# Optimization experiments

Measured on AMD Instinct MI355X. Metric: run time of the kernel, lower is better.

Reference implementation:

```python
import jax, jax.numpy as jnp
import numpy as np

B, S, C, DM, NH, DH = 1, 2048, 2048, 768, 12, 64
LN_EPS = 1e-9


def setup_inputs() -> dict:
    rng = jax.random.key(0)
    ks = jax.random.split(rng, 24)
    f32 = jnp.float32
    p = 0.02  # param init scale
    inp = {
        'query': jax.random.normal(ks[0], (B, S, DM), f32),
        'key': jax.random.normal(ks[1], (B, C, DM), f32),
        'value': jax.random.normal(ks[2], (B, C, DM), f32),
        'phi': jax.random.normal(ks[3], (S, DM), f32) * p,
        'pi': jax.random.normal(ks[4], (S, DM), f32) * p,
        'psi': jax.random.normal(ks[5], (C, DM), f32) * p,
        'omega': jax.random.normal(ks[6], (C, DM), f32) * p,
        'cls_mask': jnp.ones((S, C), f32),
        'token_type_mat': jax.random.randint(ks[7], (B, S, C), 0, 2).astype(bool),
        'attention_mask': jnp.ones((B, C), jnp.int32),
        # learned parameters
        'Wq': jax.random.normal(ks[8], (DM, NH * DH), f32) * p,
        'Wk': jax.random.normal(ks[9], (DM, NH * DH), f32) * p,
        'bk': jnp.zeros((NH * DH,), f32),
        'Wv': jax.random.normal(ks[10], (DM, NH * DH), f32) * p,
        'bv': jnp.zeros((NH * DH,), f32),
        'r_w_bias': jax.random.normal(ks[11], (NH, DH), f32) * p,
        'r_r_bias': jax.random.normal(ks[12], (NH, DH), f32) * p,
        'r_kernel': jax.random.normal(ks[13], (DM, NH, DH), f32) * p,
        'r_s_bias': jax.random.normal(ks[14], (NH, DH), f32) * p,
        'seg_embed': jax.random.normal(ks[15], (2, NH, DH), f32) * p,
        'Wo': jax.random.normal(ks[16], (NH * DH, DM), f32) * p,
        'bo': jnp.zeros((DM,), f32),
        'ln_scale': jnp.ones((DM,), f32),
        'ln_bias': jnp.zeros((DM,), f32),
    }
    return inp


def reference(query, key, value, phi, pi, psi, omega, cls_mask,
              token_type_mat, attention_mask,
              Wq, Wk, bk, Wv, bv, r_w_bias, r_r_bias, r_kernel,
              r_s_bias, seg_embed, Wo, bo, ln_scale, ln_bias):
    b, s, _ = query.shape
    c = key.shape[1]
    scale = 1.0 / DH ** 0.5
    # head projections
    q = (query @ Wq).reshape(b, s, NH, DH) * scale          # [b,i,n,h]
    k = (key @ Wk + bk).reshape(b, c, NH, DH)                # [b,j,n,h]
    v = (value @ Wv + bv).reshape(b, c, NH, DH)
    # content score
    content = jnp.einsum('binh,bjnh->bnij', q + r_w_bias * scale, k)
    # factorized relative positional attention
    qr = jnp.einsum('binh,dnh->bind', q + r_r_bias * scale, r_kernel)  # [b,i,n,d_model]
    pos = (jnp.einsum('bind,jd->bnij', qr * phi[:, None], psi)
           + jnp.einsum('bind,jd->bnij', qr * pi[:, None], omega))
    pos = pos * cls_mask
    # token-type attention
    tt_bias = jnp.einsum('binh,snh->bnis', q + r_s_bias * scale, seg_embed)  # [b,n,i,2]
    diff_tt, same_tt = jnp.split(tt_bias, 2, axis=-1)  # each [b,n,i,1]
    tt = jnp.where(token_type_mat[:, None], same_tt, diff_tt) * cls_mask
    # combine, mask, softmax
    score = content + pos + tt
    score = score - 1000000.0 * (1.0 - attention_mask[:, None, None].astype(jnp.float32))
    prob = jax.nn.softmax(score, axis=-1)  # [b,n,i,j]
    attn_vec = jnp.einsum('bnij,bjnh->binh', prob, v).reshape(b, s, NH * DH)
    attn_out = attn_vec @ Wo + bo
    # residual + layernorm
    x = query + attn_out
    mu = x.mean(-1, keepdims=True)
    var = x.var(-1, keepdims=True)
    return (x - mu) * jax.lax.rsqrt(var + LN_EPS) * ln_scale + ln_bias
```

## Files before the change

kernel.cpp:

```cpp
#include <hip/hip_runtime.h>
#include <hip/hip_bf16.h>
#include <stddef.h>

#define DEVINL __device__ __forceinline__

typedef __attribute__((ext_vector_type(8))) short short8;
typedef __attribute__((ext_vector_type(4))) float f32x4;

static constexpr int S_LEN = 2048;
static constexpr int C_LEN = 2048;
static constexpr int DMODEL = 768;
static constexpr int NHEAD = 12;
static constexpr int DHEAD = 64;
static constexpr float SCALE = 0.125f;

DEVINL float bf2f(short s) {
    union { unsigned u; float f; } v;
    v.u = ((unsigned)(unsigned short)s) << 16;
    return v.f;
}
DEVINL short f2bf(float f) {
    union { float f; unsigned u; } v;
    v.f = f;
    unsigned r = v.u + 0x7FFFu + ((v.u >> 16) & 1u);
    return (short)(r >> 16);
}
DEVINL f32x4 zero4() { f32x4 z; z[0]=0.f; z[1]=0.f; z[2]=0.f; z[3]=0.f; return z; }

DEVINL int swz(int width, int row, int col) {
    return (row * width + col) ^ ((row & 7) << 3);
}

DEVINL void gl_lds16(const short* g, short* l) {
    __builtin_amdgcn_global_load_lds(
        (const __attribute__((address_space(1))) void*)g,
        (__attribute__((address_space(3))) void*)l,
        16, 0, 0);
}

template<int ROWS, int WIDTH>
DEVINL void stage_lds_swz(short* lds_tile, const short* src, int src_stride, int w, int lane) {
    constexpr int CPR = WIDTH / 8;
    constexpr int CH  = ROWS * CPR;
    for (int c0 = w * 64; c0 < CH; c0 += 256) {
        int chunk = c0 + lane;
        int row   = chunk / CPR;
        int ccol  = chunk % CPR;
        int scol  = ccol ^ (row & 7);
        gl_lds16(src + (size_t)row * src_stride + scol * 8, lds_tile + c0 * 8);
    }
}

DEVINL void stage_addcol(short* dst, const short* src, const float* p1, const float* p2,
                         int col0, int src_stride) {
    for (int c = threadIdx.x; c < 1024; c += 256) {
        int row = c >> 3;
        int cc  = (c & 7) * 8;
        short8 a = *(const short8*)(src + (size_t)row * src_stride + cc);
        short8 r;
#pragma unroll
        for (int e = 0; e < 8; ++e)
            r[e] = f2bf(bf2f(a[e]) + (p1[col0 + cc + e] - p2[col0 + cc + e]) * SCALE);
        *(short8*)(dst + swz(64, row, cc)) = r;
    }
}

DEVINL void mfma_step_128(const short* As, const short* Bs, f32x4 acc[4][4],
                          int wr, int wc, int lane) {
#pragma unroll
    for (int kk = 0; kk < 64; kk += 32) {
        short8 a[4], b[4];
#pragma unroll
        for (int mi = 0; mi < 4; ++mi)
            a[mi] = *(const short8*)(As + swz(64, wr*64 + mi*16 + (lane & 15), kk + (lane >> 4) * 8));
#pragma unroll
        for (int ni = 0; ni < 4; ++ni)
            b[ni] = *(const short8*)(Bs + swz(64, wc*64 + ni*16 + (lane & 15), kk + (lane >> 4) * 8));
#pragma unroll
        for (int mi = 0; mi < 4; ++mi)
#pragma unroll
            for (int ni = 0; ni < 4; ++ni)
                acc[mi][ni] = __builtin_amdgcn_mfma_f32_16x16x32_bf16(a[mi], b[ni], acc[mi][ni], 0, 0, 0);
    }
}

DEVINL void mfma_row16(const short* As, const short* Bs, f32x4 acc[8], int w, int lane) {
#pragma unroll
    for (int kk = 0; kk < 64; kk += 32) {
        short8 a = *(const short8*)(As + swz(64, w*16 + (lane & 15), kk + (lane >> 4) * 8));
#pragma unroll
        for (int nj = 0; nj < 8; ++nj) {
            short8 b = *(const short8*)(Bs + swz(64, nj*16 + (lane & 15), kk + (lane >> 4) * 8));
            acc[nj] = __builtin_amdgcn_mfma_f32_16x16x32_bf16(a, b, acc[nj], 0, 0, 0);
        }
    }
}

template<int KSTEPS>
DEVINL void gemm128_body(const short* A, const short* Bt, short* As, short* Bs,
                         f32x4 acc[4][4], int wr, int wc, int lane, int w) {
    for (int ks = 0; ks < KSTEPS; ++ks) {
        if (ks) __syncthreads();
        stage_lds_swz<128, 64>(As, A + ks * 64, DMODEL, w, lane);
        stage_lds_swz<128, 64>(Bs, Bt + ks * 64, DMODEL, w, lane);
        __syncthreads();
        mfma_step_128(As, Bs, acc, wr, wc, lane);
    }
}

__global__ void conv_kernel(const float* q, const float* k, const float* v,
                            const float* psi, const float* omega, const float* rk,
                            short* qc, short* kc, short* vc,
                            short* psc, short* omc, short* rkc) {
    int z = blockIdx.z;
    const float* src; short* dst; int n4;
    switch (z) {
        case 0: src = q;     dst = qc;  n4 = 393216; break;
        case 1: src = k;     dst = kc;  n4 = 393216; break;
        case 2: src = v;     dst = vc;  n4 = 393216; break;
        case 3: src = psi;   dst = psc; n4 = 393216; break;
        case 4: src = omega; dst = omc; n4 = 393216; break;
        default: src = rk;   dst = rkc; n4 = 147456; break;
    }
    for (int i = blockIdx.x * 256 + threadIdx.x; i < n4; i += gridDim.x * 256) {
        float4 f = *(const float4*)(src + (size_t)i * 4);
        short4 o;
        o.x = f2bf(f.x); o.y = f2bf(f.y); o.z = f2bf(f.z); o.w = f2bf(f.w);
        *(short4*)(dst + (size_t)i * 4) = o;
    }
}

__global__ void transpose_kernel(const float* wq, const float* wk, const float* wv, const float* wo,
                                 short* wqt, short* wkt, short* wvt, short* wot) {
    __shared__ float tile[64][65];
    int z = blockIdx.z;
    const float* src = (z == 0) ? wq : (z == 1) ? wk : (z == 2) ? wv : wo;
    short*       dst = (z == 0) ? wqt : (z == 1) ? wkt : (z == 2) ? wvt : wot;
    int r0 = blockIdx.x * 64, c0 = blockIdx.y * 64;
    for (int e = threadIdx.x; e < 4096; e += 256) {
        int rr = e >> 6, cc = e & 63;
        tile[rr][cc] = src[(size_t)(r0 + rr) * DMODEL + c0 + cc];
    }
    __syncthreads();
    for (int e = threadIdx.x; e < 4096; e += 256) {
        int rr = e >> 6, cc = e & 63;
        dst[(size_t)(c0 + rr) * DMODEL + r0 + cc] = f2bf(tile[cc][rr]);
    }
}

__global__ __launch_bounds__(256, 2)
void qkv_kernel(const short* qc, const short* kc, const short* vc,
                const short* wqt, const short* wkt, const short* wvt,
                const float* bk, const float* bv, const float* rw,
                short* qw_a, short* kpack, short* vt) {
    __shared__ short As[128 * 64], Bs[128 * 64];
    int z = blockIdx.z;
    const short* A  = (z == 0) ? qc  : (z == 1) ? kc  : vc;
    const short* Bt = (z == 0) ? wqt : (z == 1) ? wkt : wvt;
    int i0 = blockIdx.x * 128, c0 = blockIdx.y * 128;
    int t = threadIdx.x, lane = t & 63, w = t >> 6, wr = w >> 1, wc = w & 1;

    f32x4 acc[4][4];
#pragma unroll
    for (int mi = 0; mi < 4; ++mi)
#pragma unroll
        for (int ni = 0; ni < 4; ++ni) acc[mi][ni] = zero4();

    gemm128_body<12>(A + (size_t)i0 * DMODEL, Bt + (size_t)c0 * DMODEL, As, Bs, acc, wr, wc, lane, w);

#pragma unroll
    for (int mi = 0; mi < 4; ++mi)
#pragma unroll
        for (int ni = 0; ni < 4; ++ni)
#pragma unroll
            for (int r = 0; r < 4; ++r) {
                int row = i0 + wr*64 + mi*16 + ((lane >> 4) << 2) + r;
                int col = c0 + wc*64 + ni*16 + (lane & 15);
                float v = acc[mi][ni][r];
                if (z == 0) {
                    qw_a[(size_t)row * DMODEL + col] = f2bf(v * SCALE + rw[col] * SCALE);
                } else if (z == 1) {
                    float vv = v + bk[col];
                    kpack[((size_t)(col >> 6) * C_LEN + row) * DHEAD + (col & 63)] = f2bf(vv);
                } else {
                    float vv = v + bv[col];
                    vt[((size_t)(col >> 6) * DHEAD + (col & 63)) * C_LEN + row] = f2bf(vv);
                }
            }
}

__global__ __launch_bounds__(256, 2)
void qr_kernel(const short* qwa, const short* rkc, const float* rr, const float* rw,
               const float* phi, const float* pi_, short* a1, short* a2, int n_base) {
    __shared__ short As[128 * 64], Bs[128 * 64];
    int nl = blockIdx.z, n = n_base + nl;
    int i0 = blockIdx.x * 128, d0 = blockIdx.y * 128;
    int t = threadIdx.x, lane = t & 63, w = t >> 6, wr = w >> 1, wc = w & 1;

    f32x4 acc[4][4];
#pragma unroll
    for (int mi = 0; mi < 4; ++mi)
#pragma unroll
        for (int ni = 0; ni < 4; ++ni) acc[mi][ni] = zero4();

    stage_addcol(As, qwa + (size_t)i0 * DMODEL + n * DHEAD, rr, rw, n * DHEAD, DMODEL);
    stage_lds_swz<128, 64>(Bs, rkc + (size_t)d0 * DMODEL + n * DHEAD, DMODEL, w, lane);
    __syncthreads();
    mfma_step_128(As, Bs, acc, wr, wc, lane);

#pragma unroll
    for (int mi = 0; mi < 4; ++mi)
#pragma unroll
        for (int ni = 0; ni < 4; ++ni)
#pragma unroll
            for (int r = 0; r < 4; ++r) {
                int row = i0 + wr*64 + mi*16 + ((lane >> 4) << 2) + r;
                int col = d0 + wc*64 + ni*16 + (lane & 15);
                float v = acc[mi][ni][r];
                size_t src = (size_t)row * DMODEL + col;
                size_t dst = ((size_t)nl * S_LEN + row) * DMODEL + col;
                a1[dst] = f2bf(v * phi[src]);
                a2[dst] = f2bf(v * pi_[src]);
            }
}

__global__ void ttb_kernel(const short* qwa, const float* seg, const float* rs, const float* rw,
                           float* ttd, float* tts) {
    int idx = blockIdx.x * 256 + threadIdx.x;
    int n = idx >> 11, i = idx & 2047;
    const short* q  = qwa + (size_t)i * DMODEL + n * DHEAD;
    const float* e0 = seg + n * DHEAD;
    const float* e1 = seg + NHEAD * DHEAD + n * DHEAD;
    float s0 = 0.f, s1 = 0.f;
#pragma unroll
    for (int h = 0; h < DHEAD; ++h) {
        float qv = bf2f(q[h]) + (rs[n * DHEAD + h] - rw[n * DHEAD + h]) * SCALE;
        s0 += qv * e0[h];
        s1 += qv * e1[h];
    }
    ttd[n * S_LEN + i] = s0;
    tts[n * S_LEN + i] = s1;
}

__global__ __launch_bounds__(256, 4)
void flash_kernel(const short* qw_a, const short* kpack, const short* a1, const short* a2,
                  const short* psc, const short* omc, const float* cls_mask,
                  const int* ttmat, const int* amask, const float* ttd, const float* tts,
                  const short* vt, short* pacc, float* pm, float* pl, int n_base) {
    __shared__ short As[64 * 64];
    __shared__ short Bs[128 * 64];
    __shared__ short Ps[64 * 128];

    int nl = blockIdx.y, n = n_base + nl;
    int i0 = blockIdx.x * 64;
    int jt = blockIdx.z;
    int j0 = jt * 128;
    int t = threadIdx.x, lane = t & 63, w = t >> 6;
    int lrow = lane >> 4;
    int lcol = lane & 15;

    f32x4 acc_c[8], acc_p[8];
#pragma unroll
    for (int nj = 0; nj < 8; ++nj) { acc_c[nj] = zero4(); acc_p[nj] = zero4(); }

    stage_lds_swz<64, 64>(As, qw_a + (size_t)i0 * DMODEL + n * DHEAD, DMODEL, w, lane);
    stage_lds_swz<128, 64>(Bs, kpack + ((size_t)n * C_LEN + j0) * DHEAD, DHEAD, w, lane);
    __syncthreads();
    mfma_row16(As, Bs, acc_c, w, lane);

    for (int ks = 0; ks < 24; ++ks) {
        int d0 = (ks % 12) * 64;
        const short* asrc = ((ks < 12) ? a1 : a2) + ((size_t)nl * S_LEN + i0) * DMODEL + d0;
        const short* bsrc = ((ks < 12) ? psc : omc) + (size_t)j0 * DMODEL + d0;
        __syncthreads();
        stage_lds_swz<64, 64>(As, asrc, DMODEL, w, lane);
        stage_lds_swz<128, 64>(Bs, bsrc, DMODEL, w, lane);
        __syncthreads();
        mfma_row16(As, Bs, acc_p, w, lane);
    }

    int iBase = i0 + w*16 + lrow*4;
    float tdiff[4], tsame[4];
#pragma unroll
    for (int r = 0; r < 4; ++r) {
        tdiff[r] = ttd[n * S_LEN + iBase + r];
        tsame[r] = tts[n * S_LEN + iBase + r];
    }
    float pbuf[8][4];
    float m[4] = { -1.0e9f, -1.0e9f, -1.0e9f, -1.0e9f };
#pragma unroll
    for (int nj = 0; nj < 8; ++nj) {
        int jg = j0 + nj*16 + lcol;
        float pen = 1.0e6f * (1.0f - (float)amask[jg]);
#pragma unroll
        for (int r = 0; r < 4; ++r) {
            size_t eidx = (size_t)(iBase + r) * C_LEN + jg;
            float clsv = cls_mask[eidx];
            float ttv  = ttmat[eidx] ? tsame[r] : tdiff[r];
            float sc = acc_c[nj][r] + clsv * (acc_p[nj][r] + ttv) - pen;
            pbuf[nj][r] = sc;
            m[r] = fmaxf(m[r], sc);
        }
    }
#pragma unroll
    for (int r = 0; r < 4; ++r) {
        float v = m[r];
        v = fmaxf(v, __shfl_xor(v, 1));
        v = fmaxf(v, __shfl_xor(v, 2));
        v = fmaxf(v, __shfl_xor(v, 4));
        v = fmaxf(v, __shfl_xor(v, 8));
        m[r] = v;
    }
    float l[4] = { 0.f, 0.f, 0.f, 0.f };
#pragma unroll
    for (int nj = 0; nj < 8; ++nj)
#pragma unroll
        for (int r = 0; r < 4; ++r) {
            float pv = __expf(fminf(pbuf[nj][r] - m[r], 0.0f));
            pbuf[nj][r] = pv;
            l[r] += pv;
        }
#pragma unroll
    for (int r = 0; r < 4; ++r) {
        float v = l[r];
        v += __shfl_xor(v, 1);
        v += __shfl_xor(v, 2);
        v += __shfl_xor(v, 4);
        v += __shfl_xor(v, 8);
        l[r] = v;
    }

#pragma unroll
    for (int nj = 0; nj < 8; ++nj)
#pragma unroll
        for (int r = 0; r < 4; ++r)
            Ps[swz(128, w*16 + lrow*4 + r, nj*16 + lcol)] = f2bf(pbuf[nj][r]);

    __syncthreads();
    stage_lds_swz<64, 128>(Bs, vt + (size_t)(n * DHEAD) * C_LEN + j0, C_LEN, w, lane);
    __syncthreads();

    f32x4 out_acc[4];
#pragma unroll
    for (int x = 0; x < 4; ++x) out_acc[x] = zero4();
#pragma unroll
    for (int kk = 0; kk < 4; ++kk) {
        short8 pa = *(const short8*)(Ps + swz(128, w*16 + lcol, kk*32 + lrow*8));
#pragma unroll
        for (int nh = 0; nh < 4; ++nh) {
            short8 vb = *(const short8*)(Bs + swz(128, nh*16 + lcol, kk*32 + lrow*8));
            out_acc[nh] = __builtin_amdgcn_mfma_f32_16x16x32_bf16(pa, vb, out_acc[nh], 0, 0, 0);
        }
    }

#pragma unroll
    for (int r = 0; r < 4; ++r) {
        int ig = i0 + w*16 + lrow*4 + r;
        size_t base = ((size_t)(nl * S_LEN + ig) * 16 + jt);
        if (lcol == 0) { pm[base] = m[r]; pl[base] = l[r]; }
#pragma unroll
        for (int nh = 0; nh < 4; ++nh)
            pacc[base * 64 + nh*16 + lcol] = f2bf(out_acc[nh][r]);
    }
}

__global__ void combine_kernel(const short* pacc, const float* pm, const float* pl,
                               short* avec, int n_base) {
    int idx = blockIdx.x * 256 + threadIdx.x;
    int h8 = idx & 7;
    int rest = idx >> 3;
    int i  = rest & 2047;
    int nl = rest >> 11;
    size_t b = ((size_t)nl * S_LEN + i) * 16;
    float M = -1.0e30f;
#pragma unroll
    for (int p = 0; p < 16; ++p) M = fmaxf(M, pm[b + p]);
    float L = 0.f;
    float o[8] = {0.f,0.f,0.f,0.f,0.f,0.f,0.f,0.f};
#pragma unroll
    for (int p = 0; p < 16; ++p) {
        float wg = __expf(pm[b + p] - M);
        L += wg * pl[b + p];
        short8 v = *(const short8*)(pacc + (b + p) * 64 + h8 * 8);
#pragma unroll
        for (int e = 0; e < 8; ++e) o[e] += wg * bf2f(v[e]);
    }
    float invL = 1.0f / L;
    short8 r;
#pragma unroll
    for (int e = 0; e < 8; ++e) r[e] = f2bf(o[e] * invL);
    *(short8*)(avec + (size_t)i * DMODEL + (n_base + nl) * DHEAD + h8 * 8) = r;
}

__global__ __launch_bounds__(256, 2)
void outproj_kernel(const short* avec, const short* wot, const float* bo,
                    const float* query, float* X) {
    __shared__ short As[128 * 64], Bs[128 * 64];
    int i0 = blockIdx.x * 128, c0 = blockIdx.y * 128;
    int t = threadIdx.x, lane = t & 63, w = t >> 6, wr = w >> 1, wc = w & 1;

    f32x4 acc[4][4];
#pragma unroll
    for (int mi = 0; mi < 4; ++mi)
#pragma unroll
        for (int ni = 0; ni < 4; ++ni) acc[mi][ni] = zero4();

    gemm128_body<12>(avec + (size_t)i0 * DMODEL, wot + (size_t)c0 * DMODEL, As, Bs, acc, wr, wc, lane, w);

#pragma unroll
    for (int mi = 0; mi < 4; ++mi)
#pragma unroll
        for (int ni = 0; ni < 4; ++ni)
#pragma unroll
            for (int r = 0; r < 4; ++r) {
                int row = i0 + wr*64 + mi*16 + ((lane >> 4) << 2) + r;
                int col = c0 + wc*64 + ni*16 + (lane & 15);
                float v = acc[mi][ni][r] + bo[col];
                X[(size_t)row * DMODEL + col] = v + query[(size_t)row * DMODEL + col];
            }
}

__global__ void ln_kernel(const float* X, const float* gam, const float* bet, float* out) {
    int row = blockIdx.x, t = threadIdx.x;
    const float* xr = X + (size_t)row * DMODEL;
    float x0 = xr[t], x1 = xr[t + 256], x2 = xr[t + 512];
    float s = x0 + x1 + x2;
    float q = x0*x0 + x1*x1 + x2*x2;
#pragma unroll
    for (int d = 1; d < 64; d <<= 1) { s += __shfl_xor(s, d); q += __shfl_xor(q, d); }
    __shared__ float rs_[4], rq_[4];
    int w = t >> 6, lane = t & 63;
    if (lane == 0) { rs_[w] = s; rq_[w] = q; }
    __syncthreads();
    s = rs_[0] + rs_[1] + rs_[2] + rs_[3];
    q = rq_[0] + rq_[1] + rq_[2] + rq_[3];
    float mu  = s * (1.0f / 768.0f);
    float var = q * (1.0f / 768.0f) - mu * mu;
    float rstd = rsqrtf(fmaxf(var, 0.0f) + 1e-9f);
    out[(size_t)row * DMODEL + t]       = (x0 - mu) * rstd * gam[t]       + bet[t];
    out[(size_t)row * DMODEL + t + 256] = (x1 - mu) * rstd * gam[t + 256] + bet[t + 256];
    out[(size_t)row * DMODEL + t + 512] = (x2 - mu) * rstd * gam[t + 512] + bet[t + 512];
}

extern "C" void kernel_launch(void* const* d_in, const int* in_sizes, int n_in,
                              void* d_out, int out_size, void* d_ws, size_t ws_size,
                              hipStream_t stream) {
    const float* query = (const float*)d_in[0];
    const float* key   = (const float*)d_in[1];
    const float* value = (const float*)d_in[2];
    const float* phi   = (const float*)d_in[3];
    const float* pi_   = (const float*)d_in[4];
    const float* psi   = (const float*)d_in[5];
    const float* omega = (const float*)d_in[6];
    const float* cls   = (const float*)d_in[7];
    const int*   ttm   = (const int*)d_in[8];
    const int*   am    = (const int*)d_in[9];
    const float* Wq    = (const float*)d_in[10];
    const float* Wk    = (const float*)d_in[11];
    const float* bk    = (const float*)d_in[12];
    const float* Wv    = (const float*)d_in[13];
    const float* bv    = (const float*)d_in[14];
    const float* rw    = (const float*)d_in[15];
    const float* rr    = (const float*)d_in[16];
    const float* rk    = (const float*)d_in[17];
    const float* rs    = (const float*)d_in[18];
    const float* seg   = (const float*)d_in[19];
    const float* Wo    = (const float*)d_in[20];
    const float* bo    = (const float*)d_in[21];
    const float* lng   = (const float*)d_in[22];
    const float* lnb   = (const float*)d_in[23];

    char* ws = (char*)d_ws;
    constexpr size_t SZ_W   = 768ull * 768 * 2;
    constexpr size_t SZ_SD  = 2048ull * 768 * 2;
    constexpr size_t SZ_3H  = 3ull * 2048 * 768 * 2;
    constexpr size_t OFF_WQT = 0;
    constexpr size_t OFF_WKT = OFF_WQT + SZ_W;
    constexpr size_t OFF_WVT = OFF_WKT + SZ_W;
    constexpr size_t OFF_WOT = OFF_WVT + SZ_W;
    constexpr size_t OFF_RKC = OFF_WOT + SZ_W;
    constexpr size_t OFF_QC  = OFF_RKC + SZ_W;
    constexpr size_t OFF_KC  = OFF_QC  + SZ_SD;
    constexpr size_t OFF_VC  = OFF_KC  + SZ_SD;
    constexpr size_t OFF_PSC = OFF_VC  + SZ_SD;
    constexpr size_t OFF_OMC = OFF_PSC + SZ_SD;
    constexpr size_t OFF_QWA = OFF_OMC + SZ_SD;
    constexpr size_t OFF_KP  = OFF_QWA + SZ_SD;
    constexpr size_t OFF_VT  = OFF_KP  + SZ_SD;
    constexpr size_t OFF_A1  = OFF_VT  + SZ_SD;
    constexpr size_t OFF_A2  = OFF_A1  + SZ_3H;
    constexpr size_t OFF_TTD = OFF_A2  + SZ_3H;
    constexpr size_t OFF_TTS = OFF_TTD + 12ull * 2048 * 4;
    constexpr size_t OFF_AV  = OFF_TTS + 12ull * 2048 * 4;
    constexpr size_t OFF_PA  = OFF_AV  + SZ_SD;
    constexpr size_t OFF_PM  = OFF_PA  + 3ull * 2048 * 16 * 64 * 2;
    constexpr size_t OFF_PL  = OFF_PM  + 3ull * 2048 * 16 * 4;
    constexpr size_t OFF_X   = OFF_PA;
    constexpr size_t NEED    = OFF_PL + 3ull * 2048 * 16 * 4;

    if (ws_size < NEED) return;

    short* wqt  = (short*)(ws + OFF_WQT);
    short* wkt  = (short*)(ws + OFF_WKT);
    short* wvt  = (short*)(ws + OFF_WVT);
    short* wot  = (short*)(ws + OFF_WOT);
    short* rkc  = (short*)(ws + OFF_RKC);
    short* qc   = (short*)(ws + OFF_QC);
    short* kc   = (short*)(ws + OFF_KC);
    short* vc   = (short*)(ws + OFF_VC);
    short* psc  = (short*)(ws + OFF_PSC);
    short* omc  = (short*)(ws + OFF_OMC);
    short* qwa  = (short*)(ws + OFF_QWA);
    short* kp   = (short*)(ws + OFF_KP);
    short* vt   = (short*)(ws + OFF_VT);
    short* a1   = (short*)(ws + OFF_A1);
    short* a2   = (short*)(ws + OFF_A2);
    float* ttd  = (float*)(ws + OFF_TTD);
    float* tts  = (float*)(ws + OFF_TTS);
    short* avec = (short*)(ws + OFF_AV);
    short* pacc = (short*)(ws + OFF_PA);
    float* pm   = (float*)(ws + OFF_PM);
    float* pl   = (float*)(ws + OFF_PL);
    float* X    = (float*)(ws + OFF_X);

    conv_kernel<<<dim3(768, 1, 6), 256, 0, stream>>>(query, key, value, psi, omega, rk,
                                                     qc, kc, vc, psc, omc, rkc);
    transpose_kernel<<<dim3(12, 12, 4), 256, 0, stream>>>(Wq, Wk, Wv, Wo, wqt, wkt, wvt, wot);
    qkv_kernel<<<dim3(16, 6, 3), 256, 0, stream>>>(qc, kc, vc, wqt, wkt, wvt,
                                                   bk, bv, rw, qwa, kp, vt);
    ttb_kernel<<<96, 256, 0, stream>>>(qwa, seg, rs, rw, ttd, tts);
    for (int nb = 0; nb < NHEAD; nb += 3) {
        qr_kernel<<<dim3(16, 6, 3), 256, 0, stream>>>(qwa, rkc, rr, rw, phi, pi_, a1, a2, nb);
        flash_kernel<<<dim3(32, 3, 16), 256, 0, stream>>>(qwa, kp, a1, a2, psc, omc, cls,
                                                          ttm, am, ttd, tts, vt, pacc, pm, pl, nb);
        combine_kernel<<<192, 256, 0, stream>>>(pacc, pm, pl, avec, nb);
    }
    outproj_kernel<<<dim3(16, 6), 256, 0, stream>>>(avec, wot, bo, query, X);
    ln_kernel<<<2048, 256, 0, stream>>>(X, lng, lnb, (float*)d_out);
}
```

Measured before the change: 458.4 us.

## Double-buffer flash kernel LDS staging and remap blocks for XCD locality

The flash kernel's K-loop now uses two LDS buffers, so global loads for the next stage are issued while the current stage's MFMAs run. Explicit vmcnt waits and barriers replace the full syncthreads pairs, and the V tile is prefetched during the last iteration. The grid is flattened to 1D and block ids are remapped so consecutive blocks on the same XCD share tiles. Launch bounds drop from 4 to 2 blocks per CU because LDS use grows, trading occupancy for overlap.

Result: slower. 546.3 us (+19.2%).

```diff
diff --git a/kernel.cpp b/kernel.cpp
--- a/kernel.cpp
+++ b/kernel.cpp
@@ -242,19 +242,23 @@
     tts[n * S_LEN + i] = s1;
 }
 
-__global__ __launch_bounds__(256, 4)
+__global__ __launch_bounds__(256, 2)
 void flash_kernel(const short* qw_a, const short* kpack, const short* a1, const short* a2,
                   const short* psc, const short* omc, const float* cls_mask,
                   const int* ttmat, const int* amask, const float* ttd, const float* tts,
                   const short* vt, short* pacc, float* pm, float* pl, int n_base) {
-    __shared__ short As[64 * 64];
-    __shared__ short Bs[128 * 64];
+    __shared__ short dbuf[2 * 12288];
     __shared__ short Ps[64 * 128];
 
-    int nl = blockIdx.y, n = n_base + nl;
-    int i0 = blockIdx.x * 64;
-    int jt = blockIdx.z;
+    int orig = blockIdx.x;
+    int sid  = (orig & 7) * 192 + (orig >> 3);
+    int jt = sid & 15;
+    int q6 = sid >> 4;
+    int nl = q6 % 3;
+    int i0 = (q6 / 3) * 64;
+    int n  = n_base + nl;
     int j0 = jt * 128;
+
     int t = threadIdx.x, lane = t & 63, w = t >> 6;
     int lrow = lane >> 4;
     int lcol = lane & 15;
@@ -263,20 +267,44 @@
 #pragma unroll
     for (int nj = 0; nj < 8; ++nj) { acc_c[nj] = zero4(); acc_p[nj] = zero4(); }
 
-    stage_lds_swz<64, 64>(As, qw_a + (size_t)i0 * DMODEL + n * DHEAD, DMODEL, w, lane);
-    stage_lds_swz<128, 64>(Bs, kpack + ((size_t)n * C_LEN + j0) * DHEAD, DHEAD, w, lane);
-    __syncthreads();
-    mfma_row16(As, Bs, acc_c, w, lane);
-
-    for (int ks = 0; ks < 24; ++ks) {
-        int d0 = (ks % 12) * 64;
-        const short* asrc = ((ks < 12) ? a1 : a2) + ((size_t)nl * S_LEN + i0) * DMODEL + d0;
-        const short* bsrc = ((ks < 12) ? psc : omc) + (size_t)j0 * DMODEL + d0;
-        __syncthreads();
-        stage_lds_swz<64, 64>(As, asrc, DMODEL, w, lane);
-        stage_lds_swz<128, 64>(Bs, bsrc, DMODEL, w, lane);
-        __syncthreads();
-        mfma_row16(As, Bs, acc_p, w, lane);
+    const short* a_base = a1 + ((size_t)nl * S_LEN + i0) * DMODEL;
+    const short* a2base = a2 + ((size_t)nl * S_LEN + i0) * DMODEL;
+    const short* p_base = psc + (size_t)j0 * DMODEL;
+    const short* o_base = omc + (size_t)j0 * DMODEL;
+
+    auto STAGE = [&](int b, int s) {
+        short* B = dbuf + b * 12288;
+        if (s == 0) {
+            stage_lds_swz<64, 64>(B, qw_a + (size_t)i0 * DMODEL + n * DHEAD, DMODEL, w, lane);
+            stage_lds_swz<128, 64>(B + 4096, kpack + ((size_t)n * C_LEN + j0) * DHEAD, DHEAD, w, lane);
+        } else {
+            int d0 = ((s - 1) % 12) * 64;
+            const short* asrc = ((s <= 12) ? a_base : a2base) + d0;
+            const short* bsrc = ((s <= 12) ? p_base : o_base) + d0;
+            stage_lds_swz<64, 64>(B, asrc, DMODEL, w, lane);
+            stage_lds_swz<128, 64>(B + 4096, bsrc, DMODEL, w, lane);
+        }
+    };
+
+    STAGE(0, 0);
+    STAGE(1, 1);
+
+    for (int ks = 0; ks < 25; ++ks) {
+        int cur = ks & 1;
+        short* B = dbuf + cur * 12288;
+        if (ks < 24) { asm volatile("s_waitcnt vmcnt(6)" ::: "memory"); }
+        else         { asm volatile("s_waitcnt vmcnt(4)" ::: "memory"); }
+        __builtin_amdgcn_sched_barrier(0);
+        __builtin_amdgcn_s_barrier();
+        if (ks == 0) mfma_row16(B, B + 4096, acc_c, w, lane);
+        else         mfma_row16(B, B + 4096, acc_p, w, lane);
+        asm volatile("s_waitcnt lgkmcnt(0)" ::: "memory");
+        __builtin_amdgcn_sched_barrier(0);
+        __builtin_amdgcn_s_barrier();
+        if (ks < 23)
+            STAGE(cur, ks + 2);
+        else if (ks == 23)
+            stage_lds_swz<64, 128>(dbuf + 12288, vt + (size_t)(n * DHEAD) * C_LEN + j0, C_LEN, w, lane);
     }
 
     int iBase = i0 + w*16 + lrow*4;
@@ -337,8 +365,6 @@
             Ps[swz(128, w*16 + lrow*4 + r, nj*16 + lcol)] = f2bf(pbuf[nj][r]);
 
     __syncthreads();
-    stage_lds_swz<64, 128>(Bs, vt + (size_t)(n * DHEAD) * C_LEN + j0, C_LEN, w, lane);
-    __syncthreads();
 
     f32x4 out_acc[4];
 #pragma unroll
@@ -348,7 +374,7 @@
         short8 pa = *(const short8*)(Ps + swz(128, w*16 + lcol, kk*32 + lrow*8));
 #pragma unroll
         for (int nh = 0; nh < 4; ++nh) {
-            short8 vb = *(const short8*)(Bs + swz(128, nh*16 + lcol, kk*32 + lrow*8));
+            short8 vb = *(const short8*)(dbuf + 12288 + swz(128, nh*16 + lcol, kk*32 + lrow*8));
             out_acc[nh] = __builtin_amdgcn_mfma_f32_16x16x32_bf16(pa, vb, out_acc[nh], 0, 0, 0);
         }
     }
@@ -531,8 +557,8 @@
     ttb_kernel<<<96, 256, 0, stream>>>(qwa, seg, rs, rw, ttd, tts);
     for (int nb = 0; nb < NHEAD; nb += 3) {
         qr_kernel<<<dim3(16, 6, 3), 256, 0, stream>>>(qwa, rkc, rr, rw, phi, pi_, a1, a2, nb);
-        flash_kernel<<<dim3(32, 3, 16), 256, 0, stream>>>(qwa, kp, a1, a2, psc, omc, cls,
-                                                          ttm, am, ttd, tts, vt, pacc, pm, pl, nb);
+        flash_kernel<<<dim3(1536), 256, 0, stream>>>(qwa, kp, a1, a2, psc, omc, cls,
+                                                     ttm, am, ttd, tts, vt, pacc, pm, pl, nb);
         combine_kernel<<<192, 256, 0, stream>>>(pacc, pm, pl, avec, nb);
     }
     outproj_kernel<<<dim3(16, 6), 256, 0, stream>>>(avec, wot, bo, query, X);
```
